# Optimization experiments

Hardware: AMD Instinct MI355X
Metric: run time of the kernel (lower is better)

## Reference

```python
import jax, jax.numpy as jnp
import numpy as np
import math

NEG = -1000000.0


def setup_inputs() -> dict:
    key = jax.random.key(0)
    ks = jax.random.split(key, 8)
    B, S, D = 4, 2048, 1024
    std = 1.0 / math.sqrt(D)
    return {
        "queries": jax.random.normal(ks[0], (B, S, D), jnp.float32),
        "keys": jax.random.normal(ks[1], (B, S, D), jnp.float32),
        "values": jax.random.normal(ks[2], (B, S, D), jnp.float32),
        "valid_len": jax.random.randint(ks[3], (B,), 1, S, dtype=jnp.int64 if jax.config.jax_enable_x64 else jnp.int32),
        "W_q": jax.random.normal(ks[4], (D, D), jnp.float32) * std,
        "W_k": jax.random.normal(ks[5], (D, D), jnp.float32) * std,
        "W_v": jax.random.normal(ks[6], (D, D), jnp.float32) * std,
        "W_o": jax.random.normal(ks[7], (D, D), jnp.float32) * std,
    }


def reference(queries, keys, values, valid_len, W_q, W_k, W_v, W_o):
    NUM_HEADS = 16
    B, S, D = queries.shape
    hd = D // NUM_HEADS

    def split_heads(x):
        # (B, S, D) -> (B, H, S, hd)
        return x.reshape(B, -1, NUM_HEADS, hd).transpose(0, 2, 1, 3)

    # nn.Linear with weight W applies x @ W.T
    q = split_heads(queries @ W_q.T)
    k = split_heads(keys @ W_k.T)
    v = split_heads(values @ W_v.T)

    scale = 1.0 / math.sqrt(hd)
    scores = jnp.einsum('bhqd,bhkd->bhqk', q, k) * scale  # (B, H, Sq, Sk)

    # key-padding mask from valid_len: positions >= valid_len are masked
    kpos = jnp.arange(scores.shape[-1])
    pad_mask = kpos[None, None, None, :] >= valid_len[:, None, None, None]
    scores = jnp.where(pad_mask, NEG, scores)
    attn = jax.nn.softmax(scores, axis=-1)

    out = jnp.einsum('bhqk,bhkd->bhqd', attn, v)  # (B, H, Sq, hd)
    out = out.transpose(0, 2, 1, 3).reshape(B, -1, D)
    return out @ W_o.T
```

## Files before the change

### kernel.cpp

```cpp
#include <hip/hip_runtime.h>
#include <hip/hip_bf16.h>

using bf16_t = __bf16;
using bf16x8 = __attribute__((ext_vector_type(8))) __bf16;
using bf16x4 = __attribute__((ext_vector_type(4))) __bf16;
using bf16x2 = __attribute__((ext_vector_type(2))) __bf16;
using f32x4  = __attribute__((ext_vector_type(4))) float;

#define S_  2048
#define D_  1024

typedef __attribute__((address_space(1))) unsigned int glb_u32;
typedef __attribute__((address_space(3))) unsigned int lds_u32;

__device__ __forceinline__ void async_cp16(const void* g, void* lds) {
    __builtin_amdgcn_global_load_lds(
        (glb_u32*)(unsigned long long)g,
        (lds_u32*)(unsigned int)(unsigned long long)lds,
        16, 0, 0);
}

__global__ __launch_bounds__(256) void cast4_f32_bf16(const float* __restrict__ a, const float* __restrict__ b,
                                                      const float* __restrict__ c, const float* __restrict__ dd,
                                                      bf16_t* __restrict__ oa, bf16_t* __restrict__ ob,
                                                      bf16_t* __restrict__ oc, bf16_t* __restrict__ od, int n4) {
    int i = blockIdx.x * 256 + threadIdx.x;
    if (i >= n4) return;
    const float* s; bf16_t* d;
    int w = blockIdx.y;
    if      (w == 0) { s = a;  d = oa; }
    else if (w == 1) { s = b;  d = ob; }
    else if (w == 2) { s = c;  d = oc; }
    else             { s = dd; d = od; }
    float4 f = reinterpret_cast<const float4*>(s)[i];
    bf16x4 o;
    o[0] = (bf16_t)f.x; o[1] = (bf16_t)f.y; o[2] = (bf16_t)f.z; o[3] = (bf16_t)f.w;
    reinterpret_cast<bf16x4*>(d)[i] = o;
}

__global__ __launch_bounds__(256) void qkv_gemm(const float* __restrict__ qf,
                                                const float* __restrict__ kf,
                                                const float* __restrict__ vf,
                                                const bf16_t* __restrict__ Wqb,
                                                const bf16_t* __restrict__ Wkb,
                                                const bf16_t* __restrict__ Wvb,
                                                bf16_t* __restrict__ Qp,
                                                bf16_t* __restrict__ Kp,
                                                bf16_t* __restrict__ Vt,
                                                float cs) {
    __shared__ bf16_t As[2][128 * 32];
    __shared__ bf16_t Bs[2][128 * 32];
    const int K = 1024;
    int tid  = threadIdx.x;
    int lane = tid & 63;
    int w    = tid >> 6;
    int l15  = lane & 15, quad = lane >> 4;

    int bid = blockIdx.x;
    int xcd = bid & 7, idx = bid >> 3;
    int z   = idx >> 6;
    int rem = idx & 63;
    int m0 = (xcd * 8 + (rem & 7)) * 128;
    int n0 = (rem >> 3) * 128;
    int wm = (w >> 1) * 64, wn = (w & 1) * 64;

    const float*  Af; const bf16_t* Bt;
    if      (z == 0) { Af = qf; Bt = Wqb; }
    else if (z == 1) { Af = kf; Bt = Wkb; }
    else             { Af = vf; Bt = Wvb; }
    float scale = (z == 0) ? cs : 1.0f;

    const float*  Ag = Af + (size_t)(m0 + (tid >> 2)) * K + (tid & 3) * 8;
    const bf16_t* Bg = Bt + (size_t)(n0 + (tid >> 2)) * K + (tid & 3) * 8;

    float4 a0, a1, a2, a3;
    auto loadA = [&](int k0) {
        const float* p = Ag + k0;
        a0 = *reinterpret_cast<const float4*>(p);
        a1 = *reinterpret_cast<const float4*>(p + 4);
        a2 = *reinterpret_cast<const float4*>(p + (size_t)64 * K);
        a3 = *reinterpret_cast<const float4*>(p + (size_t)64 * K + 4);
    };
    auto storeA = [&](bf16_t* dst) {
        bf16x8 o0, o1;
        o0[0] = (bf16_t)a0.x; o0[1] = (bf16_t)a0.y; o0[2] = (bf16_t)a0.z; o0[3] = (bf16_t)a0.w;
        o0[4] = (bf16_t)a1.x; o0[5] = (bf16_t)a1.y; o0[6] = (bf16_t)a1.z; o0[7] = (bf16_t)a1.w;
        o1[0] = (bf16_t)a2.x; o1[1] = (bf16_t)a2.y; o1[2] = (bf16_t)a2.z; o1[3] = (bf16_t)a2.w;
        o1[4] = (bf16_t)a3.x; o1[5] = (bf16_t)a3.y; o1[6] = (bf16_t)a3.z; o1[7] = (bf16_t)a3.w;
        *reinterpret_cast<bf16x8*>(dst + tid * 8)        = o0;
        *reinterpret_cast<bf16x8*>(dst + tid * 8 + 2048) = o1;
    };

    f32x4 acc[4][4] = {};

    loadA(0);
    async_cp16(Bg,                  &Bs[0][tid * 8]);
    async_cp16(Bg + (size_t)64 * K, &Bs[0][tid * 8 + 2048]);
    storeA(As[0]);
    __syncthreads();

    for (int k0 = 0; k0 < K; k0 += 32) {
        int cur = (k0 >> 5) & 1;
        bool more = (k0 + 32 < K);
        if (more) {
            int nxt = cur ^ 1;
            loadA(k0 + 32);
            async_cp16(Bg + k0 + 32,                  &Bs[nxt][tid * 8]);
            async_cp16(Bg + k0 + 32 + (size_t)64 * K, &Bs[nxt][tid * 8 + 2048]);
        }
        bf16x8 af[4], bfr[4];
#pragma unroll
        for (int t = 0; t < 4; t++) {
            af[t]  = *reinterpret_cast<const bf16x8*>(&As[cur][(wm + t * 16 + l15) * 32 + quad * 8]);
            bfr[t] = *reinterpret_cast<const bf16x8*>(&Bs[cur][(wn + t * 16 + l15) * 32 + quad * 8]);
        }
#pragma unroll
        for (int mt = 0; mt < 4; mt++)
#pragma unroll
            for (int nt = 0; nt < 4; nt++)
                acc[mt][nt] = __builtin_amdgcn_mfma_f32_16x16x32_bf16(af[mt], bfr[nt], acc[mt][nt], 0, 0, 0);
        if (more) storeA(As[cur ^ 1]);
        __syncthreads();
    }

    if (z == 2) {
#pragma unroll
        for (int mt = 0; mt < 4; mt++)
#pragma unroll
            for (int nt = 0; nt < 4; nt++) {
                int m = m0 + wm + mt * 16 + quad * 4;
                int n = n0 + wn + nt * 16 + l15;
                bf16x4 o4;
#pragma unroll
                for (int r = 0; r < 4; r++) o4[r] = (bf16_t)acc[mt][nt][r];
                size_t vrow = (size_t)((m >> 11) * 16 + (n >> 6)) * 64 + (n & 63);
                int ml = m & 2047;
                int mp = (ml & ~31) | (((ml >> 2) & 3) << 3) | (((ml >> 4) & 1) << 2);
                *reinterpret_cast<bf16x4*>(&Vt[vrow * S_ + mp]) = o4;
            }
    } else {
        bf16_t* Co = (z == 0) ? Qp : Kp;
#pragma unroll
        for (int mt = 0; mt < 4; mt++)
#pragma unroll
            for (int nt = 0; nt < 4; nt++)
#pragma unroll
                for (int r = 0; r < 4; r++) {
                    int m = m0 + wm + mt * 16 + quad * 4 + r;
                    int n = n0 + wn + nt * 16 + l15;
                    Co[(size_t)m * 1024 + n] = (bf16_t)(acc[mt][nt][r] * scale);
                }
    }
}

__global__ __launch_bounds__(256) void gemm_out(const bf16_t* __restrict__ A,
                                                const bf16_t* __restrict__ Bt,
                                                float* __restrict__ C) {
    __shared__ bf16_t As[2][128 * 32];
    __shared__ bf16_t Bs[2][128 * 32];
    const int K = 1024;
    int tid  = threadIdx.x;
    int lane = tid & 63;
    int w    = tid >> 6;
    int l15  = lane & 15, quad = lane >> 4;

    int bid = blockIdx.x;
    int xcd = bid & 7, idx = bid >> 3;
    int m0 = (xcd * 8 + (idx & 7)) * 128;
    int n0 = (idx >> 3) * 128;
    int wm = (w >> 1) * 64, wn = (w & 1) * 64;

    const bf16_t* Ag = A  + (size_t)(m0 + (tid >> 2)) * K + (tid & 3) * 8;
    const bf16_t* Bg = Bt + (size_t)(n0 + (tid >> 2)) * K + (tid & 3) * 8;

    f32x4 acc[4][4] = {};

    async_cp16(Ag,                  &As[0][tid * 8]);
    async_cp16(Ag + (size_t)64 * K, &As[0][tid * 8 + 2048]);
    async_cp16(Bg,                  &Bs[0][tid * 8]);
    async_cp16(Bg + (size_t)64 * K, &Bs[0][tid * 8 + 2048]);
    __syncthreads();

    for (int k0 = 0; k0 < K; k0 += 32) {
        int cur = (k0 >> 5) & 1;
        if (k0 + 32 < K) {
            int nxt = cur ^ 1;
            async_cp16(Ag + k0 + 32,                  &As[nxt][tid * 8]);
            async_cp16(Ag + k0 + 32 + (size_t)64 * K, &As[nxt][tid * 8 + 2048]);
            async_cp16(Bg + k0 + 32,                  &Bs[nxt][tid * 8]);
            async_cp16(Bg + k0 + 32 + (size_t)64 * K, &Bs[nxt][tid * 8 + 2048]);
        }
        bf16x8 af[4], bfr[4];
#pragma unroll
        for (int t = 0; t < 4; t++) {
            af[t]  = *reinterpret_cast<const bf16x8*>(&As[cur][(wm + t * 16 + l15) * 32 + quad * 8]);
            bfr[t] = *reinterpret_cast<const bf16x8*>(&Bs[cur][(wn + t * 16 + l15) * 32 + quad * 8]);
        }
#pragma unroll
        for (int mt = 0; mt < 4; mt++)
#pragma unroll
            for (int nt = 0; nt < 4; nt++)
                acc[mt][nt] = __builtin_amdgcn_mfma_f32_16x16x32_bf16(af[mt], bfr[nt], acc[mt][nt], 0, 0, 0);
        __syncthreads();
    }

#pragma unroll
    for (int mt = 0; mt < 4; mt++)
#pragma unroll
        for (int nt = 0; nt < 4; nt++)
#pragma unroll
            for (int r = 0; r < 4; r++) {
                int m = m0 + wm + mt * 16 + quad * 4 + r;
                int n = n0 + wn + nt * 16 + l15;
                C[(size_t)m * 1024 + n] = acc[mt][nt][r];
            }
}

__global__ __launch_bounds__(256) void attn_fused(const bf16_t* __restrict__ Qp,
                                                  const bf16_t* __restrict__ Kp,
                                                  const bf16_t* __restrict__ Vt,
                                                  const int* __restrict__ vlen_p,
                                                  bf16_t* __restrict__ Out) {
    __shared__ bf16_t smem[4][64 * 64];

    int tid  = threadIdx.x;
    int lane = tid & 63, w = tid >> 6;
    int l15  = lane & 15, quad = lane >> 4;

    int nk[4], ord[4] = {0, 1, 2, 3};
#pragma unroll
    for (int i = 0; i < 4; i++) nk[i] = (vlen_p[i] + 63) >> 6;
#pragma unroll
    for (int i = 0; i < 3; i++)
#pragma unroll
        for (int j = 0; j < 3 - i; j++)
            if (nk[ord[j + 1]] > nk[ord[j]]) { int t = ord[j]; ord[j] = ord[j + 1]; ord[j + 1] = t; }

    int bid  = blockIdx.x;
    int b    = ord[bid >> 9];
    int t    = bid & 511;
    int h    = (t & 7) * 2 + ((t >> 3) & 1);
    int qblk = t >> 4;
    int vlen = vlen_p[b];
    int nkb  = (vlen + 63) >> 6;

    const bf16_t* Qg = Qp + (size_t)(b * S_ + qblk * 64) * D_ + h * 64;
    const bf16_t* Kg = Kp + (size_t)b * S_ * D_ + h * 64;
    const bf16_t* Vg = Vt + (size_t)(b * 16 + h) * 64 * S_;

    int r0 = tid >> 3, s0 = tid & 7;
    int sx = (s0 ^ (r0 & 7)) * 8;
    const bf16_t* kS0 = Kg + (size_t)r0 * D_ + sx;
    const bf16_t* kS1 = kS0 + (size_t)32 * D_;
    const bf16_t* vS0 = Vg + (size_t)r0 * S_ + sx;
    const bf16_t* vS1 = vS0 + (size_t)32 * S_;

    {
        const bf16_t* qS0 = Qg + (size_t)r0 * D_ + sx;
        async_cp16(qS0,                   smem[2] + tid * 8);
        async_cp16(qS0 + (size_t)32 * D_, smem[2] + tid * 8 + 2048);
        async_cp16(kS0, smem[0] + tid * 8);
        async_cp16(kS1, smem[0] + tid * 8 + 2048);
        async_cp16(vS0, smem[1] + tid * 8);
        async_cp16(vS1, smem[1] + tid * 8 + 2048);
    }
    __syncthreads();

    bf16x8 qf[2];
    {
        int row = w * 16 + l15, x = row & 7;
#pragma unroll
        for (int kk = 0; kk < 2; kk++)
            qf[kk] = *reinterpret_cast<const bf16x8*>(&smem[2][row * 64 + ((kk * 4 + quad) ^ x) * 8]);
    }
    __syncthreads();

    f32x4 o[4] = {};
    float l_st = 0.f;

    for (int kb = 0; kb < nkb; kb++) {
        int cur = kb & 1;
        if (kb + 1 < nkb) {
            int nxt = cur ^ 1;
            kS0 += (size_t)64 * D_; kS1 += (size_t)64 * D_;
            vS0 += 64;              vS1 += 64;
            async_cp16(kS0, smem[nxt * 2]     + tid * 8);
            async_cp16(kS1, smem[nxt * 2]     + tid * 8 + 2048);
            async_cp16(vS0, smem[nxt * 2 + 1] + tid * 8);
            async_cp16(vS1, smem[nxt * 2 + 1] + tid * 8 + 2048);
        }
        const bf16_t* Kc = smem[cur * 2];
        const bf16_t* Vc = smem[cur * 2 + 1];

        f32x4 sc[4] = {};
#pragma unroll
        for (int nt = 0; nt < 4; nt++) {
            int row = nt * 16 + l15, x = row & 7;
#pragma unroll
            for (int kk = 0; kk < 2; kk++) {
                bf16x8 kf = *reinterpret_cast<const bf16x8*>(&Kc[row * 64 + ((kk * 4 + quad) ^ x) * 8]);
                sc[nt] = __builtin_amdgcn_mfma_f32_16x16x32_bf16(kf, qf[kk], sc[nt], 0, 0, 0);
            }
        }

        bool partial = (vlen & 63) && (kb == nkb - 1);
        bf16x8 pf[2];
        float lacc = 0.f;
        if (!partial) {
#pragma unroll
            for (int nt = 0; nt < 4; nt++)
#pragma unroll
                for (int r = 0; r < 4; r++) {
                    float p = __builtin_exp2f(sc[nt][r]);
                    lacc += p;
                    pf[nt >> 1][(nt & 1) * 4 + r] = (bf16_t)p;
                }
        } else {
#pragma unroll
            for (int nt = 0; nt < 4; nt++)
#pragma unroll
                for (int r = 0; r < 4; r++) {
                    float p = __builtin_exp2f(sc[nt][r]);
                    if (kb * 64 + nt * 16 + quad * 4 + r >= vlen) p = 0.f;
                    lacc += p;
                    pf[nt >> 1][(nt & 1) * 4 + r] = (bf16_t)p;
                }
        }
        l_st += lacc;

#pragma unroll
        for (int np = 0; np < 2; np++)
#pragma unroll
            for (int dt = 0; dt < 4; dt++) {
                int row = dt * 16 + l15, x = row & 7;
                bf16x8 vfr = *reinterpret_cast<const bf16x8*>(&Vc[row * 64 + ((np * 4 + quad) ^ x) * 8]);
                o[dt] = __builtin_amdgcn_mfma_f32_16x16x32_bf16(vfr, pf[np], o[dt], 0, 0, 0);
            }

        __syncthreads();
    }

    float l = l_st;
    l += __shfl_xor(l, 16);
    l += __shfl_xor(l, 32);
    float inv = 1.0f / l;

    bf16_t* T = smem[0];
    {
        int row = w * 16 + l15, x = row & 7;
#pragma unroll
        for (int dt = 0; dt < 4; dt++) {
            bf16x4 o4;
#pragma unroll
            for (int r = 0; r < 4; r++) o4[r] = (bf16_t)(o[dt][r] * inv);
            int slot = dt * 2 + (quad >> 1);
            *reinterpret_cast<bf16x4*>(&T[row * 64 + (slot ^ x) * 8 + (quad & 1) * 4]) = o4;
        }
    }
    __syncthreads();
    {
        int row = tid >> 2, ch = tid & 3, x = row & 7;
        size_t obase = (size_t)(b * S_ + qblk * 64 + row) * D_ + h * 64 + ch * 16;
        bf16x8 f0 = *reinterpret_cast<const bf16x8*>(&T[row * 64 + ((ch * 2)     ^ x) * 8]);
        bf16x8 f1 = *reinterpret_cast<const bf16x8*>(&T[row * 64 + ((ch * 2 + 1) ^ x) * 8]);
        *reinterpret_cast<bf16x8*>(&Out[obase])     = f0;
        *reinterpret_cast<bf16x8*>(&Out[obase + 8]) = f1;
    }
}

extern "C" void kernel_launch(void* const* d_in, const int* in_sizes, int n_in,
                              void* d_out, int out_size, void* d_ws, size_t ws_size,
                              hipStream_t stream) {
    const float* q  = (const float*)d_in[0];
    const float* k  = (const float*)d_in[1];
    const float* v  = (const float*)d_in[2];
    const int*   vl = (const int*)d_in[3];
    const float* Wq = (const float*)d_in[4];
    const float* Wk = (const float*)d_in[5];
    const float* Wv = (const float*)d_in[6];
    const float* Wo = (const float*)d_in[7];
    float* out = (float*)d_out;

    bf16_t* ws = (bf16_t*)d_ws;
    const size_t SD = (size_t)8192 * 1024;
    const size_t WW = (size_t)1024 * 1024;
    bf16_t* tmpB = ws + SD;
    bf16_t* Qp   = ws + 2 * SD;
    bf16_t* Kp   = ws + 3 * SD;
    bf16_t* Vt   = ws + 4 * SD;
    bf16_t* Wqb  = ws + 5 * SD;
    bf16_t* Wkb  = Wqb + WW;
    bf16_t* Wvb  = Wqb + 2 * WW;
    bf16_t* Wob  = Wqb + 3 * WW;

    const float cs = 0.18033688f;
    dim3 blk(256);

    cast4_f32_bf16<<<dim3(1024, 4), blk, 0, stream>>>(Wq, Wk, Wv, Wo, Wqb, Wkb, Wvb, Wob, 262144);
    qkv_gemm<<<dim3(1536), blk, 0, stream>>>(q, k, v, Wqb, Wkb, Wvb, Qp, Kp, Vt, cs);
    attn_fused<<<dim3(2048), blk, 0, stream>>>(Qp, Kp, Vt, vl, tmpB);
    gemm_out<<<dim3(512), blk, 0, stream>>>(tmpB, Wob, out);
}
```

Baseline: 322.1 us.

## Triple-buffer LDS pipelines with vmcnt waits and XOR-swizzle GEMM tiles

The output GEMM and the attention kernel move from double-buffered LDS with full __syncthreads to a three-stage ring. Each iteration waits with an explicit s_waitcnt vmcnt and one barrier, so two tiles stay in flight during compute. The QKV and output GEMMs also XOR-swizzle their LDS tile layouts to cut bank conflicts on fragment reads. Attention now loads Q fragments straight from global memory into registers, which drops an LDS staging round. The cost is more LDS per block, which may lower occupancy, and the counted waits rely on a fixed number of outstanding loads per stage.

After: 331.4 us. 2.9% more time.

```diff
diff --git a/kernel.cpp b/kernel.cpp
--- a/kernel.cpp
+++ b/kernel.cpp
@@ -4,7 +4,6 @@
 using bf16_t = __bf16;
 using bf16x8 = __attribute__((ext_vector_type(8))) __bf16;
 using bf16x4 = __attribute__((ext_vector_type(4))) __bf16;
-using bf16x2 = __attribute__((ext_vector_type(2))) __bf16;
 using f32x4  = __attribute__((ext_vector_type(4))) float;
 
 #define S_  2048
@@ -70,8 +69,20 @@
     else             { Af = vf; Bt = Wvb; }
     float scale = (z == 0) ? cs : 1.0f;
 
-    const float*  Ag = Af + (size_t)(m0 + (tid >> 2)) * K + (tid & 3) * 8;
-    const bf16_t* Bg = Bt + (size_t)(n0 + (tid >> 2)) * K + (tid & 3) * 8;
+    const float* Ag = Af + (size_t)(m0 + (tid >> 2)) * K + (tid & 3) * 8;
+
+    int arow = tid >> 2, aslot = tid & 3;
+    int aoff = arow * 32 + ((aslot ^ ((arow >> 1) & 3)) * 8);
+
+    const bf16_t* bSrc[2]; bf16_t* bDst0[2], *bDst1[2];
+#pragma unroll
+    for (int j = 0; j < 2; j++) {
+        int linear = j * 256 + tid;
+        int row = linear >> 2, s = linear & 3;
+        bSrc[j]  = Bt + (size_t)(n0 + row) * K + ((s ^ ((row >> 1) & 3)) * 8);
+        bDst0[j] = &Bs[0][linear * 8];
+        bDst1[j] = &Bs[1][linear * 8];
+    }
 
     float4 a0, a1, a2, a3;
     auto loadA = [&](int k0) {
@@ -87,15 +98,15 @@
         o0[4] = (bf16_t)a1.x; o0[5] = (bf16_t)a1.y; o0[6] = (bf16_t)a1.z; o0[7] = (bf16_t)a1.w;
         o1[0] = (bf16_t)a2.x; o1[1] = (bf16_t)a2.y; o1[2] = (bf16_t)a2.z; o1[3] = (bf16_t)a2.w;
         o1[4] = (bf16_t)a3.x; o1[5] = (bf16_t)a3.y; o1[6] = (bf16_t)a3.z; o1[7] = (bf16_t)a3.w;
-        *reinterpret_cast<bf16x8*>(dst + tid * 8)        = o0;
-        *reinterpret_cast<bf16x8*>(dst + tid * 8 + 2048) = o1;
+        *reinterpret_cast<bf16x8*>(dst + aoff)        = o0;
+        *reinterpret_cast<bf16x8*>(dst + aoff + 2048) = o1;
     };
 
     f32x4 acc[4][4] = {};
 
     loadA(0);
-    async_cp16(Bg,                  &Bs[0][tid * 8]);
-    async_cp16(Bg + (size_t)64 * K, &Bs[0][tid * 8 + 2048]);
+    async_cp16(bSrc[0], bDst0[0]);
+    async_cp16(bSrc[1], bDst0[1]);
     storeA(As[0]);
     __syncthreads();
 
@@ -105,14 +116,16 @@
         if (more) {
             int nxt = cur ^ 1;
             loadA(k0 + 32);
-            async_cp16(Bg + k0 + 32,                  &Bs[nxt][tid * 8]);
-            async_cp16(Bg + k0 + 32 + (size_t)64 * K, &Bs[nxt][tid * 8 + 2048]);
+            async_cp16(bSrc[0] + k0 + 32, nxt ? bDst1[0] : bDst0[0]);
+            async_cp16(bSrc[1] + k0 + 32, nxt ? bDst1[1] : bDst0[1]);
         }
         bf16x8 af[4], bfr[4];
 #pragma unroll
         for (int t = 0; t < 4; t++) {
-            af[t]  = *reinterpret_cast<const bf16x8*>(&As[cur][(wm + t * 16 + l15) * 32 + quad * 8]);
-            bfr[t] = *reinterpret_cast<const bf16x8*>(&Bs[cur][(wn + t * 16 + l15) * 32 + quad * 8]);
+            int ra = wm + t * 16 + l15;
+            int rb = wn + t * 16 + l15;
+            af[t]  = *reinterpret_cast<const bf16x8*>(&As[cur][ra * 32 + ((quad ^ ((ra >> 1) & 3)) * 8)]);
+            bfr[t] = *reinterpret_cast<const bf16x8*>(&Bs[cur][rb * 32 + ((quad ^ ((rb >> 1) & 3)) * 8)]);
         }
 #pragma unroll
         for (int mt = 0; mt < 4; mt++)
@@ -156,8 +169,8 @@
 __global__ __launch_bounds__(256) void gemm_out(const bf16_t* __restrict__ A,
                                                 const bf16_t* __restrict__ Bt,
                                                 float* __restrict__ C) {
-    __shared__ bf16_t As[2][128 * 32];
-    __shared__ bf16_t Bs[2][128 * 32];
+    __shared__ bf16_t As[3][128 * 32];
+    __shared__ bf16_t Bs[3][128 * 32];
     const int K = 1024;
     int tid  = threadIdx.x;
     int lane = tid & 63;
@@ -170,38 +183,53 @@
     int n0 = (idx >> 3) * 128;
     int wm = (w >> 1) * 64, wn = (w & 1) * 64;
 
-    const bf16_t* Ag = A  + (size_t)(m0 + (tid >> 2)) * K + (tid & 3) * 8;
-    const bf16_t* Bg = Bt + (size_t)(n0 + (tid >> 2)) * K + (tid & 3) * 8;
+    const bf16_t* aSrc[2]; const bf16_t* bSrc[2];
+    int dOff[2];
+#pragma unroll
+    for (int j = 0; j < 2; j++) {
+        int linear = j * 256 + tid;
+        int row = linear >> 2, s = linear & 3;
+        int sw = (s ^ ((row >> 1) & 3)) * 8;
+        aSrc[j] = A  + (size_t)(m0 + row) * K + sw;
+        bSrc[j] = Bt + (size_t)(n0 + row) * K + sw;
+        dOff[j] = linear * 8;
+    }
+
+    auto stage = [&](int buf, int koff) {
+#pragma unroll
+        for (int j = 0; j < 2; j++) async_cp16(aSrc[j] + koff, &As[buf][dOff[j]]);
+#pragma unroll
+        for (int j = 0; j < 2; j++) async_cp16(bSrc[j] + koff, &Bs[buf][dOff[j]]);
+    };
 
     f32x4 acc[4][4] = {};
 
-    async_cp16(Ag,                  &As[0][tid * 8]);
-    async_cp16(Ag + (size_t)64 * K, &As[0][tid * 8 + 2048]);
-    async_cp16(Bg,                  &Bs[0][tid * 8]);
-    async_cp16(Bg + (size_t)64 * K, &Bs[0][tid * 8 + 2048]);
-    __syncthreads();
-
-    for (int k0 = 0; k0 < K; k0 += 32) {
-        int cur = (k0 >> 5) & 1;
-        if (k0 + 32 < K) {
-            int nxt = cur ^ 1;
-            async_cp16(Ag + k0 + 32,                  &As[nxt][tid * 8]);
-            async_cp16(Ag + k0 + 32 + (size_t)64 * K, &As[nxt][tid * 8 + 2048]);
-            async_cp16(Bg + k0 + 32,                  &Bs[nxt][tid * 8]);
-            async_cp16(Bg + k0 + 32 + (size_t)64 * K, &Bs[nxt][tid * 8 + 2048]);
-        }
+    stage(0, 0);
+    stage(1, 32);
+
+    int cur = 0, nx2 = 2;
+    for (int i = 0; i < 32; ++i) {
+        if (i == 31) asm volatile("s_waitcnt vmcnt(0)" ::: "memory");
+        else         asm volatile("s_waitcnt vmcnt(4)" ::: "memory");
+        __builtin_amdgcn_s_barrier();
+        if (i + 2 < 32) stage(nx2, (i + 2) * 32);
+
         bf16x8 af[4], bfr[4];
 #pragma unroll
         for (int t = 0; t < 4; t++) {
-            af[t]  = *reinterpret_cast<const bf16x8*>(&As[cur][(wm + t * 16 + l15) * 32 + quad * 8]);
-            bfr[t] = *reinterpret_cast<const bf16x8*>(&Bs[cur][(wn + t * 16 + l15) * 32 + quad * 8]);
+            int ra = wm + t * 16 + l15;
+            int rb = wn + t * 16 + l15;
+            af[t]  = *reinterpret_cast<const bf16x8*>(&As[cur][ra * 32 + ((quad ^ ((ra >> 1) & 3)) * 8)]);
+            bfr[t] = *reinterpret_cast<const bf16x8*>(&Bs[cur][rb * 32 + ((quad ^ ((rb >> 1) & 3)) * 8)]);
         }
 #pragma unroll
         for (int mt = 0; mt < 4; mt++)
 #pragma unroll
             for (int nt = 0; nt < 4; nt++)
                 acc[mt][nt] = __builtin_amdgcn_mfma_f32_16x16x32_bf16(af[mt], bfr[nt], acc[mt][nt], 0, 0, 0);
-        __syncthreads();
+
+        cur = (cur == 2) ? 0 : cur + 1;
+        nx2 = (nx2 == 2) ? 0 : nx2 + 1;
     }
 
 #pragma unroll
@@ -221,7 +249,7 @@
                                                   const bf16_t* __restrict__ Vt,
                                                   const int* __restrict__ vlen_p,
                                                   bf16_t* __restrict__ Out) {
-    __shared__ bf16_t smem[4][64 * 64];
+    __shared__ bf16_t smem[6][64 * 64];
 
     int tid  = threadIdx.x;
     int lane = tid & 63, w = tid >> 6;
@@ -244,53 +272,47 @@
     int vlen = vlen_p[b];
     int nkb  = (vlen + 63) >> 6;
 
-    const bf16_t* Qg = Qp + (size_t)(b * S_ + qblk * 64) * D_ + h * 64;
     const bf16_t* Kg = Kp + (size_t)b * S_ * D_ + h * 64;
     const bf16_t* Vg = Vt + (size_t)(b * 16 + h) * 64 * S_;
 
+    bf16x8 qf[2];
+    {
+        int qrow = w * 16 + l15;
+        const bf16_t* qp = Qp + (size_t)(b * S_ + qblk * 64 + qrow) * D_ + h * 64 + quad * 8;
+        qf[0] = *reinterpret_cast<const bf16x8*>(qp);
+        qf[1] = *reinterpret_cast<const bf16x8*>(qp + 32);
+    }
+
     int r0 = tid >> 3, s0 = tid & 7;
     int sx = (s0 ^ (r0 & 7)) * 8;
-    const bf16_t* kS0 = Kg + (size_t)r0 * D_ + sx;
-    const bf16_t* kS1 = kS0 + (size_t)32 * D_;
-    const bf16_t* vS0 = Vg + (size_t)r0 * S_ + sx;
-    const bf16_t* vS1 = vS0 + (size_t)32 * S_;
-
-    {
-        const bf16_t* qS0 = Qg + (size_t)r0 * D_ + sx;
-        async_cp16(qS0,                   smem[2] + tid * 8);
-        async_cp16(qS0 + (size_t)32 * D_, smem[2] + tid * 8 + 2048);
-        async_cp16(kS0, smem[0] + tid * 8);
-        async_cp16(kS1, smem[0] + tid * 8 + 2048);
-        async_cp16(vS0, smem[1] + tid * 8);
-        async_cp16(vS1, smem[1] + tid * 8 + 2048);
-    }
-    __syncthreads();
-
-    bf16x8 qf[2];
-    {
-        int row = w * 16 + l15, x = row & 7;
-#pragma unroll
-        for (int kk = 0; kk < 2; kk++)
-            qf[kk] = *reinterpret_cast<const bf16x8*>(&smem[2][row * 64 + ((kk * 4 + quad) ^ x) * 8]);
-    }
-    __syncthreads();
+    const bf16_t* kB = Kg + (size_t)r0 * D_ + sx;
+    const bf16_t* vB = Vg + (size_t)r0 * S_ + sx;
+
+    auto stage = [&](int slot, int tile) {
+        const bf16_t* kp = kB + (size_t)tile * 64 * D_;
+        const bf16_t* vp = vB + tile * 64;
+        async_cp16(kp,                    smem[slot]     + tid * 8);
+        async_cp16(kp + (size_t)32 * D_,  smem[slot]     + tid * 8 + 2048);
+        async_cp16(vp,                    smem[3 + slot] + tid * 8);
+        async_cp16(vp + (size_t)32 * S_,  smem[3 + slot] + tid * 8 + 2048);
+    };
+
+    stage(0, 0);
+    stage(1, nkb > 1 ? 1 : 0);
 
     f32x4 o[4] = {};
     float l_st = 0.f;
 
+    int cur = 0, nx2 = 2;
     for (int kb = 0; kb < nkb; kb++) {
-        int cur = kb & 1;
-        if (kb + 1 < nkb) {
-            int nxt = cur ^ 1;
-            kS0 += (size_t)64 * D_; kS1 += (size_t)64 * D_;
-            vS0 += 64;              vS1 += 64;
-            async_cp16(kS0, smem[nxt * 2]     + tid * 8);
-            async_cp16(kS1, smem[nxt * 2]     + tid * 8 + 2048);
-            async_cp16(vS0, smem[nxt * 2 + 1] + tid * 8);
-            async_cp16(vS1, smem[nxt * 2 + 1] + tid * 8 + 2048);
-        }
-        const bf16_t* Kc = smem[cur * 2];
-        const bf16_t* Vc = smem[cur * 2 + 1];
+        asm volatile("s_waitcnt vmcnt(4)" ::: "memory");
+        __builtin_amdgcn_s_barrier();
+        {
+            int tnext = kb + 2 < nkb ? kb + 2 : nkb - 1;
+            stage(nx2, tnext);
+        }
+        const bf16_t* Kc = smem[cur];
+        const bf16_t* Vc = smem[3 + cur];
 
         f32x4 sc[4] = {};
 #pragma unroll
@@ -337,7 +359,8 @@
                 o[dt] = __builtin_amdgcn_mfma_f32_16x16x32_bf16(vfr, pf[np], o[dt], 0, 0, 0);
             }
 
-        __syncthreads();
+        cur = (cur == 2) ? 0 : cur + 1;
+        nx2 = (nx2 == 2) ? 0 : nx2 + 1;
     }
 
     float l = l_st;
@@ -345,6 +368,7 @@
     l += __shfl_xor(l, 32);
     float inv = 1.0f / l;
 
+    __syncthreads();
     bf16_t* T = smem[0];
     {
         int row = w * 16 + l15, x = row & 7;
```
